# Performance work log

Hardware: AMD Instinct MI355X
Metric: run time of the kernel (lower is better)

Reference implementation:

```python
import jax, jax.numpy as jnp
import numpy as np

B, N, C = 2, 2048, 1024
H, D = 16, 64
SEQ_DROPOUT = 0.4
K_KEEP = int(N * (1.0 - SEQ_DROPOUT))  # 1228 kept keys per (b, h)


def setup_inputs() -> dict:
    key = jax.random.key(0)
    k1, k2, k3, k4, k5 = jax.random.split(key, 5)
    x = jax.random.normal(k1, (B, N, C), dtype=jnp.float32)
    W_qkv = jax.random.normal(k2, (3 * H * D, C), dtype=jnp.float32) * 0.02
    W_out = jax.random.normal(k3, (C, H * D), dtype=jnp.float32) * 0.02
    pos_bias = jax.random.normal(k4, (H, N, N), dtype=jnp.float32) * 0.1
    seq_mask = jax.random.randint(k5, (B, H, N), 0, 10, dtype=jnp.int32)
    mask = jnp.zeros((B, N), dtype=bool)  # True = padded / masked out
    return {"x": x, "W_qkv": W_qkv, "W_out": W_out, "pos_bias": pos_bias,
            "seq_mask": seq_mask, "mask": mask}


def reference(x, W_qkv, W_out, pos_bias, seq_mask, mask):
    scale = D ** -0.5
    # qkv projection: (b n (h d qkv)) -> q,k,v each [B,H,N,D]
    qkv = (x @ W_qkv.T).reshape(B, N, H, D, 3)
    q = jnp.moveaxis(qkv[..., 0], 2, 1)
    k_full = jnp.moveaxis(qkv[..., 1], 2, 1)
    v_full = jnp.moveaxis(qkv[..., 2], 2, 1)

    # random top-k key subsampling per (b, h); padded positions forced out
    sm = jnp.where(mask[:, None, :], jnp.int32(-1), seq_mask)
    _, idx = jax.lax.top_k(sm, K_KEEP)              # [B,H,K]
    idx = jnp.sort(idx, axis=-1)

    kk = jnp.take_along_axis(k_full, idx[..., None], axis=2)  # [B,H,K,D]
    vv = jnp.take_along_axis(v_full, idx[..., None], axis=2)
    k_mask = jnp.take_along_axis(jnp.broadcast_to(mask[:, None, :], (B, H, N)), idx, axis=-1)

    dots = jnp.einsum('bhid,bhjd->bhij', q, kk) * scale       # [B,H,N,K]
    # gather position bias columns at kept key indices
    pb = jnp.take_along_axis(pos_bias[None], idx[:, :, None, :], axis=-1)  # [B,H,N,K]
    dots = dots + pb

    qk_mask = jnp.logical_and(mask[:, None, :, None], k_mask[:, :, None, :])
    causal = idx[:, :, None, :] > jnp.arange(N)[None, None, :, None]
    qk_mask = jnp.logical_or(qk_mask, causal)

    dots = jnp.where(qk_mask, -jnp.finfo(dots.dtype).max, dots)
    attn = jax.nn.softmax(dots, axis=-1)
    out = jnp.einsum('bhij,bhjd->bhid', attn, vv)             # [B,H,N,D]
    out = jnp.moveaxis(out, 1, 2).reshape(B, N, H * D)
    return out @ W_out.T
```

## Files before the change

kernel.cpp:

```cpp
#include <hip/hip_runtime.h>
#include <hip/hip_bf16.h>
#include <float.h>

#define BB    2
#define NSEQ  2048
#define CDIM  1024
#define HH    16
#define DD    64
#define KKEEP 1228

typedef __attribute__((ext_vector_type(8))) short short8_t;
typedef __attribute__((ext_vector_type(4))) short short4_t;
typedef __attribute__((ext_vector_type(4))) float f32x4;
typedef __attribute__((ext_vector_type(16))) float f32x16;
typedef __attribute__((ext_vector_type(4))) float float4_t;
typedef __attribute__((ext_vector_type(4))) unsigned uint4_t;
typedef __bf16 bf16x8 __attribute__((ext_vector_type(8)));

#define Z16 ((f32x16){0.f,0.f,0.f,0.f,0.f,0.f,0.f,0.f,0.f,0.f,0.f,0.f,0.f,0.f,0.f,0.f})

static __device__ __forceinline__ short f2bf(float x) {
  __hip_bfloat16 h = __float2bfloat16(x);
  short s;
  __builtin_memcpy(&s, &h, 2);
  return s;
}

static __device__ __forceinline__ float bf2f(short s) {
  unsigned u = ((unsigned)(unsigned short)s) << 16;
  float f;
  __builtin_memcpy(&f, &u, 4);
  return f;
}

static __device__ __forceinline__ f32x4 mfma16(bf16x8 a, bf16x8 b, f32x4 c) {
  return __builtin_amdgcn_mfma_f32_16x16x32_bf16(a, b, c, 0, 0, 0);
}

static __device__ __forceinline__ f32x16 mfma32(bf16x8 a, bf16x8 b, f32x16 c) {
  return __builtin_amdgcn_mfma_f32_32x32x16_bf16(a, b, c, 0, 0, 0);
}

static __device__ __forceinline__ void gll16(const void* g, void* l) {
  __builtin_amdgcn_global_load_lds((const __attribute__((address_space(1))) void*)g,
                                   (__attribute__((address_space(3))) void*)l,
                                   16, 0, 0);
}

__global__ __launch_bounds__(256) void cast_f32_bf16_kernel(
    const float* __restrict__ src, short* __restrict__ dst, int n4) {
  int i = blockIdx.x * 256 + threadIdx.x;
  if (i >= n4) return;
  float4_t v = ((const float4_t*)src)[i];
  short4_t o;
  o[0] = f2bf(v[0]); o[1] = f2bf(v[1]); o[2] = f2bf(v[2]); o[3] = f2bf(v[3]);
  ((short4_t*)dst)[i] = o;
}

__global__ __launch_bounds__(256) void cast_wqkv_kernel(
    const float* __restrict__ w, short* __restrict__ dst) {
  int rr = blockIdx.x;
  int c = rr >> 10, hd = rr & 1023;
  int h = hd >> 6, d = hd & 63;
  int srow = h * 192 + d * 3 + c;
  int col = threadIdx.x * 4;
  float4_t v = *(const float4_t*)(w + (size_t)srow * CDIM + col);
  short4_t o;
  o[0] = f2bf(v[0]); o[1] = f2bf(v[1]); o[2] = f2bf(v[2]); o[3] = f2bf(v[3]);
  *(short4_t*)(dst + (size_t)rr * CDIM + col) = o;
}

template <int EPI>
__global__ __launch_bounds__(256) void gemm_bt_kernel(
    const short* __restrict__ A, const short* __restrict__ B, int K, int N,
    float* __restrict__ outF, short* __restrict__ outQ,
    short* __restrict__ outK, short* __restrict__ outV) {
  __shared__ __align__(16) short lA[128 * 32];
  __shared__ __align__(16) short lB[128 * 32];
  int m0 = blockIdx.y * 128, n0 = blockIdx.x * 128;
  int tid = threadIdx.x, lane = tid & 63;
  int w = tid >> 6;
  int lq = lane & 15, lg = lane >> 4;
  int wm = w >> 1, wn = w & 1;

  f32x4 acc[4][4];
#pragma unroll
  for (int m = 0; m < 4; ++m)
#pragma unroll
    for (int n = 0; n < 4; ++n) acc[m][n] = (f32x4){0.f, 0.f, 0.f, 0.f};

  const int c0 = tid, c1 = tid + 256;
  const short* Ar0 = A + (size_t)(m0 + (c0 >> 2)) * K + (c0 & 3) * 8;
  const short* Ar1 = A + (size_t)(m0 + (c1 >> 2)) * K + (c1 & 3) * 8;
  const short* Br0 = B + (size_t)(n0 + (c0 >> 2)) * K + (c0 & 3) * 8;
  const short* Br1 = B + (size_t)(n0 + (c1 >> 2)) * K + (c1 & 3) * 8;

  for (int k0 = 0; k0 < K; k0 += 32) {
    gll16(Ar0 + k0, lA + c0 * 8);
    gll16(Ar1 + k0, lA + c1 * 8);
    gll16(Br0 + k0, lB + c0 * 8);
    gll16(Br1 + k0, lB + c1 * 8);
    __syncthreads();
    bf16x8 af[4], bf[4];
#pragma unroll
    for (int m = 0; m < 4; ++m)
      af[m] = *(const bf16x8*)(lA + (wm * 64 + m * 16 + lq) * 32 + lg * 8);
#pragma unroll
    for (int n = 0; n < 4; ++n)
      bf[n] = *(const bf16x8*)(lB + (wn * 64 + n * 16 + lq) * 32 + lg * 8);
#pragma unroll
    for (int m = 0; m < 4; ++m)
#pragma unroll
      for (int n = 0; n < 4; ++n) acc[m][n] = mfma16(af[m], bf[n], acc[m][n]);
    __syncthreads();
  }

#pragma unroll
  for (int m = 0; m < 4; ++m)
#pragma unroll
    for (int n = 0; n < 4; ++n) {
      int row_b = m0 + wm * 64 + m * 16 + lg * 4;
      int col = n0 + wn * 64 + n * 16 + lq;
#pragma unroll
      for (int r = 0; r < 4; ++r) {
        float v = acc[m][n][r];
        int row = row_b + r;
        if constexpr (EPI == 1) {
          outF[(size_t)row * N + col] = v;
        } else {
          int c = col >> 10, cc = col & 1023;
          int bb2 = row >> 11, nn = row & 2047;
          int hh2 = cc >> 6, dd2 = cc & 63;
          short val = f2bf(v);
          if (c == 0)
            outQ[((size_t)(bb2 * HH + hh2) * NSEQ + nn) * DD + dd2] = val;
          else if (c == 1)
            outK[((size_t)(bb2 * HH + hh2) * NSEQ + nn) * DD + dd2] = val;
          else
            outV[((size_t)(bb2 * HH + hh2) * DD + dd2) * NSEQ + nn] = val;
        }
      }
    }
}

__global__ __launch_bounds__(256) void topk_kernel(const int* __restrict__ seq_mask,
                                                   unsigned* __restrict__ keepw,
                                                   int* __restrict__ jminb) {
  __shared__ int hist[10];
  __shared__ int vals[NSEQ];
  __shared__ int seqc[256];
  __shared__ unsigned wbuf[64];
  __shared__ int sT, sNeed, sMin;
  int bh = blockIdx.x, tid = threadIdx.x;
  if (tid < 10) hist[tid] = 0;
  if (tid < 64) wbuf[tid] = 0;
  if (tid == 0) sMin = NSEQ;
  __syncthreads();
  const int* sm = seq_mask + (size_t)bh * NSEQ;
  for (int i = tid; i < NSEQ; i += 256) {
    int v = sm[i];
    vals[i] = v;
    atomicAdd(&hist[v], 1);
  }
  __syncthreads();
  if (tid == 0) {
    int cum = 0, t = 0;
    for (int v = 9; v >= 0; --v) {
      int hv = hist[v];
      if (cum + hv >= KKEEP) { t = v; break; }
      cum += hv;
    }
    sT = t;
    sNeed = KKEEP - cum;
  }
  __syncthreads();
  int t = sT, need = sNeed;
  int base = tid * 8, leq = 0;
  int lv[8];
#pragma unroll
  for (int j = 0; j < 8; ++j) {
    lv[j] = vals[base + j];
    leq += (lv[j] == t);
  }
  seqc[tid] = leq;
  __syncthreads();
  for (int off = 1; off < 256; off <<= 1) {
    int a = 0;
    if (tid >= off) a = seqc[tid - off];
    __syncthreads();
    seqc[tid] += a;
    __syncthreads();
  }
  int eqp = seqc[tid] - leq;
  unsigned mybits = 0;
#pragma unroll
  for (int j = 0; j < 8; ++j) {
    int v = lv[j];
    bool kept = (v > t) || (v == t && eqp < need);
    if (v == t) eqp++;
    if (kept) mybits |= (1u << j);
  }
  atomicOr(&wbuf[tid >> 2], mybits << ((tid & 3) * 8));
  if (mybits) atomicMin(&sMin, base + __ffs(mybits) - 1);
  __syncthreads();
  if (tid < 64) keepw[(size_t)bh * 64 + tid] = wbuf[tid];
  if (tid == 0) jminb[bh] = sMin;
}

#define PBLOAD(SUF, T)                                                         \
  do {                                                                         \
    const float* pb_ = pbrow + (T) * 32 + hi4;                                 \
    pbg0##SUF = *(const float4_t*)(pb_);                                       \
    pbg1##SUF = *(const float4_t*)(pb_ + 8);                                   \
    pbg2##SUF = *(const float4_t*)(pb_ + 16);                                  \
    pbg3##SUF = *(const float4_t*)(pb_ + 24);                                  \
    kw##SUF = kwp[T];                                                          \
  } while (0)

#define CHUNK32(SUF, OSUF, T)                                                  \
  do {                                                                         \
    int kb0c = (T) * 32;                                                       \
    const short* kp_ = kb_bh + (size_t)(kb0c + lq32) * DD + hi8;               \
    bf16x8 k0 = *(const bf16x8*)(kp_);                                         \
    bf16x8 k1 = *(const bf16x8*)(kp_ + 16);                                    \
    bf16x8 k2 = *(const bf16x8*)(kp_ + 32);                                    \
    bf16x8 k3 = *(const bf16x8*)(kp_ + 48);                                    \
    const short* vp0_ = vT0 + kb0c + hi8;                                      \
    const short* vp1_ = vT1 + kb0c + hi8;                                      \
    bf16x8 v00 = *(const bf16x8*)(vp0_);                                       \
    bf16x8 v01 = *(const bf16x8*)(vp0_ + 16);                                  \
    bf16x8 v10 = *(const bf16x8*)(vp1_);                                       \
    bf16x8 v11 = *(const bf16x8*)(vp1_ + 16);                                  \
    if ((T) + 1 < t1) PBLOAD(OSUF, (T) + 1);                                   \
    f32x16 s = Z16;                                                            \
    s = mfma32(k0, qf0, s);                                                    \
    s = mfma32(k1, qf1, s);                                                    \
    s = mfma32(k2, qf2, s);                                                    \
    s = mfma32(k3, qf3, s);                                                    \
    float sv[16];                                                              \
    unsigned vb = 0;                                                           \
    float cm = -FLT_MAX;                                                       \
    _Pragma("unroll") for (int g = 0; g < 4; ++g) {                            \
      float4_t pbg = (g == 0) ? pbg0##SUF : (g == 1) ? pbg1##SUF               \
                   : (g == 2) ? pbg2##SUF : pbg3##SUF;                         \
      _Pragma("unroll") for (int m = 0; m < 4; ++m) {                          \
        int rr = g * 4 + m;                                                    \
        int kk = m + g * 8 + hi4;                                              \
        int jj = kb0c + kk;                                                    \
        unsigned keep = (kw##SUF >> kk) & 1u;                                  \
        float x = (keep && jj <= qglob) ? fmaf(s[rr], 0.125f, pbg[m])          \
                                        : -FLT_MAX;                            \
        vb |= keep << rr;                                                      \
        sv[rr] = x;                                                            \
        cm = fmaxf(cm, x);                                                     \
      }                                                                        \
    }                                                                          \
    if (__any(cm > mrun)) {                     \
      float rm = fmaxf(cm, __shfl_xor(cm, 32));                                \
      float mnew = fmaxf(mrun, rm);                                            \
      float fsc = __expf(mrun - mnew);                                         \
      mrun = mnew;                                                             \
      lsum *= fsc;                                                             \
      _Pragma("unroll") for (int rr = 0; rr < 16; ++rr) {                      \
        int qr = (rr & 3) + 8 * (rr >> 2) + hi4;                               \
        float fr = __shfl(fsc, qr);                                            \
        o0[rr] *= fr;                                                          \
        o1[rr] *= fr;                                                          \
      }                                                                        \
    }                                                                          \
    float pv[16];                                                              \
    float psum = 0.f;                                                          \
    _Pragma("unroll") for (int rr = 0; rr < 16; ++rr) {                        \
      float p_ = ((vb >> rr) & 1u) ? __expf(sv[rr] - mrun) : 0.f;              \
      pv[rr] = p_;                                                             \
      psum += p_;                                                              \
    }                                                                          \
    lsum += psum;                                                              \
    unsigned w0_, w1_, w2_, w3_, w4_, w5_, w6_, w7_;                           \
    asm("v_cvt_pk_bf16_f32 %0, %1, %2" : "=v"(w0_) : "v"(pv[0]), "v"(pv[1]));  \
    asm("v_cvt_pk_bf16_f32 %0, %1, %2" : "=v"(w1_) : "v"(pv[2]), "v"(pv[3]));  \
    asm("v_cvt_pk_bf16_f32 %0, %1, %2" : "=v"(w2_) : "v"(pv[4]), "v"(pv[5]));  \
    asm("v_cvt_pk_bf16_f32 %0, %1, %2" : "=v"(w3_) : "v"(pv[6]), "v"(pv[7]));  \
    asm("v_cvt_pk_bf16_f32 %0, %1, %2" : "=v"(w4_) : "v"(pv[8]), "v"(pv[9]));  \
    asm("v_cvt_pk_bf16_f32 %0, %1, %2" : "=v"(w5_) : "v"(pv[10]), "v"(pv[11]));\
    asm("v_cvt_pk_bf16_f32 %0, %1, %2" : "=v"(w6_) : "v"(pv[12]), "v"(pv[13]));\
    asm("v_cvt_pk_bf16_f32 %0, %1, %2" : "=v"(w7_) : "v"(pv[14]), "v"(pv[15]));\
       \
    asm("v_permlane32_swap_b32 %0, %1" : "+v"(w0_), "+v"(w2_));                \
    asm("v_permlane32_swap_b32 %0, %1" : "+v"(w1_), "+v"(w3_));                \
    asm("v_permlane32_swap_b32 %0, %1" : "+v"(w4_), "+v"(w6_));                \
    asm("v_permlane32_swap_b32 %0, %1" : "+v"(w5_), "+v"(w7_));                \
    uint4_t u0_ = {w0_, w1_, w2_, w3_};                                        \
    uint4_t u1_ = {w4_, w5_, w6_, w7_};                                        \
    bf16x8 pf0 = __builtin_bit_cast(bf16x8, u0_);                              \
    bf16x8 pf1 = __builtin_bit_cast(bf16x8, u1_);                              \
    o0 = mfma32(pf0, v00, o0);                                                 \
    o0 = mfma32(pf1, v01, o0);                                                 \
    o1 = mfma32(pf0, v10, o1);                                                 \
    o1 = mfma32(pf1, v11, o1);                                                 \
  } while (0)

__global__ __launch_bounds__(128) void attn_split_kernel(
    const short* __restrict__ qb, const short* __restrict__ kb,
    const short* __restrict__ vT, const unsigned* __restrict__ keepw,
    const int* __restrict__ jminb, const float* __restrict__ pos_bias,
    short* __restrict__ Opart, float* __restrict__ mlb,
    short* __restrict__ attn_out) {
  int w = threadIdx.x >> 6, lane = threadIdx.x & 63;
  int lq32 = lane & 31, hi = lane >> 5;
  int hi4 = hi * 4, hi8 = hi * 8;
  int gid = blockIdx.x * 2 + w;
  int bh = gid & 31;
  int r = gid >> 5;
  int jmin = jminb[bh];

  int tau, part, t0, t1;
  bool big;
  if (r < 32) {
    tau = 63 - r; part = 0; t0 = 0; t1 = 32; big = true;
  } else if (r < 34) {
    tau = 0; part = r - 32;
    int nkb = (jmin > 0) ? 64 : 1;
    int half = nkb >> 1;
    t0 = part ? half : 0;
    t1 = part ? nkb : half;
    big = true;
  } else if (r < 66) {
    tau = 63 - (r - 34); part = 1; t0 = 32; t1 = tau + 1; big = true;
  } else {
    tau = 31 - (r - 66); part = 0; t0 = 0;
    t1 = (tau * 32 < jmin) ? 64 : tau + 1;
    big = false;
  }
  int stile = (tau == 0) ? 32 : (tau - 32);
  int b = bh >> 4, h = bh & 15;
  int q0 = tau << 5;
  int qglob = q0 + lq32;

  const short* qp_ = qb + ((size_t)bh * NSEQ + qglob) * DD + hi8;
  bf16x8 qf0 = *(const bf16x8*)(qp_);
  bf16x8 qf1 = *(const bf16x8*)(qp_ + 16);
  bf16x8 qf2 = *(const bf16x8*)(qp_ + 32);
  bf16x8 qf3 = *(const bf16x8*)(qp_ + 48);

  const short* kb_bh = kb + (size_t)bh * NSEQ * DD;
  const short* vT0 = vT + ((size_t)bh * DD + lq32) * NSEQ;
  const short* vT1 = vT + ((size_t)bh * DD + 32 + lq32) * NSEQ;
  const float* pbrow = pos_bias + ((size_t)h * NSEQ + qglob) * NSEQ;
  const unsigned* kwp = keepw + (size_t)bh * 64;

  float mrun = -FLT_MAX, lsum = 0.f;
  f32x16 o0 = Z16, o1 = Z16;

  float4_t pbg0A, pbg1A, pbg2A, pbg3A, pbg0B, pbg1B, pbg2B, pbg3B;
  unsigned kwA, kwB;

  if (t0 < t1) {
    PBLOAD(A, t0);
    int t = t0;
    for (;;) {
      CHUNK32(A, B, t);
      if (++t >= t1) break;
      CHUNK32(B, A, t);
      if (++t >= t1) break;
    }
  }

  float ltot = lsum + __shfl_xor(lsum, 32);

  if (big) {
    int sidx = ((bh * 33 + stile) << 1) + part;
    if (hi == 0) {
      mlb[(size_t)sidx * 64 + lq32] = mrun;
      mlb[(size_t)sidx * 64 + 32 + lq32] = ltot;
    }
    short* op = Opart + (size_t)sidx * 2048;
#pragma unroll
    for (int rr = 0; rr < 16; ++rr) {
      int qr = (rr & 3) + 8 * (rr >> 2) + hi4;
      op[qr * 64 + lq32]      = f2bf(o0[rr]);
      op[qr * 64 + 32 + lq32] = f2bf(o1[rr]);
    }
  } else {
    float inv = 1.f / ltot;
    short* ob = attn_out + ((size_t)b * NSEQ + q0) * CDIM + h * DD + lq32;
#pragma unroll
    for (int rr = 0; rr < 16; ++rr) {
      int qr = (rr & 3) + 8 * (rr >> 2) + hi4;
      float ir = __shfl(inv, qr);
      short* orow = ob + (size_t)qr * CDIM;
      orow[0]  = f2bf(o0[rr] * ir);
      orow[32] = f2bf(o1[rr] * ir);
    }
  }
}

__global__ __launch_bounds__(64) void combine_kernel(
    const float* __restrict__ mlb, const short* __restrict__ Opart,
    short* __restrict__ attn_out) {
  int blk = blockIdx.x;
  int bh = blk & 31, st = blk >> 5;
  int tau = (st < 32) ? (st + 32) : 0;
  int b = bh >> 4, h = bh & 15;
  int lane = threadIdx.x;
  int q = lane >> 1, d0 = (lane & 1) * 32;
  int p0 = (bh * 33 + st) << 1, p1 = p0 + 1;
  float m0 = mlb[(size_t)p0 * 64 + q], l0 = mlb[(size_t)p0 * 64 + 32 + q];
  float m1 = mlb[(size_t)p1 * 64 + q], l1 = mlb[(size_t)p1 * 64 + 32 + q];
  float M = fmaxf(m0, m1);
  float f0 = __expf(m0 - M), f1 = __expf(m1 - M);
  float L = l0 * f0 + l1 * f1;
  float inv = 1.f / L;
  const short* q0p = Opart + (size_t)p0 * 2048 + q * 64 + d0;
  const short* q1p = Opart + (size_t)p1 * 2048 + q * 64 + d0;
  short* orow = attn_out + ((size_t)b * NSEQ + tau * 32 + q) * CDIM + h * DD + d0;
#pragma unroll
  for (int c = 0; c < 4; ++c) {
    short8_t x0 = *(const short8_t*)(q0p + c * 8);
    short8_t x1 = *(const short8_t*)(q1p + c * 8);
    short8_t oo;
#pragma unroll
    for (int jj = 0; jj < 8; ++jj) {
      float a = bf2f(x0[jj]) * f0 + bf2f(x1[jj]) * f1;
      oo[jj] = f2bf(a * inv);
    }
    *(short8_t*)(orow + c * 8) = oo;
  }
}

extern "C" void kernel_launch(void* const* d_in, const int* in_sizes, int n_in,
                              void* d_out, int out_size, void* d_ws, size_t ws_size,
                              hipStream_t stream) {
  const float* x        = (const float*)d_in[0];
  const float* Wqkv     = (const float*)d_in[1];
  const float* Wout     = (const float*)d_in[2];
  const float* pos_bias = (const float*)d_in[3];
  const int*   seq_mask = (const int*)d_in[4];
  float* out = (float*)d_out;

  char* ws = (char*)d_ws;
  short* qb    = (short*)(ws);
  short* kbuf  = (short*)(ws + ((size_t)8  << 20));
  short* vTb   = (short*)(ws + ((size_t)16 << 20));
  short* woutb = (short*)(ws + ((size_t)24 << 20));
  short* xb    = (short*)(ws + ((size_t)26 << 20));
  short* aob   = (short*)(ws + ((size_t)26 << 20));
  short* wqkvb = (short*)(ws + ((size_t)34 << 20));
  short* Opart = (short*)(ws + ((size_t)34 << 20));
  float* mlb   = (float*)(ws + ((size_t)43 << 20));
  unsigned* keepw = (unsigned*)(ws + ((size_t)44 << 20));
  int* jminb   = (int*)(ws + ((size_t)44 << 20) + 65536);

  cast_f32_bf16_kernel<<<4096, 256, 0, stream>>>(x, xb, (BB * NSEQ * CDIM) / 4);
  cast_wqkv_kernel<<<3072, 256, 0, stream>>>(Wqkv, wqkvb);
  cast_f32_bf16_kernel<<<1024, 256, 0, stream>>>(Wout, woutb, (CDIM * HH * DD) / 4);

  gemm_bt_kernel<0><<<dim3(24, 32), 256, 0, stream>>>(xb, wqkvb, CDIM, 3 * HH * DD,
                                                      nullptr, qb, kbuf, vTb);

  topk_kernel<<<BB * HH, 256, 0, stream>>>(seq_mask, keepw, jminb);

  attn_split_kernel<<<1552, 128, 0, stream>>>(qb, kbuf, vTb, keepw, jminb,
                                              pos_bias, Opart, mlb, aob);

  combine_kernel<<<1056, 64, 0, stream>>>(mlb, Opart, aob);

  gemm_bt_kernel<1><<<dim3(8, 32), 256, 0, stream>>>(aob, woutb, HH * DD, CDIM,
                                                     out, nullptr, nullptr, nullptr);
}
```

Baseline: 209.0 us.

## Pre-swizzle K/V into MFMA fragment layout and rebalance split-K attention partitions

The QKV GEMM epilogue now writes K and V straight into a per-32-key-chunk layout that matches the MFMA operand fragments, so attention loads become contiguous per-lane 16-byte reads. Attention work is also re-split: each query tile is cut into 2–4 key partitions depending on its causal length, giving 2848 more even work items instead of a mix of big and small ones. Every tile now goes through a generalized combine kernel that merges up to 4 partials. This adds more partial-output traffic and a combine pass over all tiles, in exchange for better load balance and coalesced loads.

```diff
diff --git a/kernel.cpp b/kernel.cpp
--- a/kernel.cpp
+++ b/kernel.cpp
@@ -46,6 +46,14 @@
                                    (__attribute__((address_space(3))) void*)l,
                                    16, 0, 0);
 }
+
+static __device__ __forceinline__ int soff(int tau) {
+  if (tau == 0) return 0;
+  if (tau < 32) return 4 + (tau - 1) * 2;
+  if (tau < 48) return 66 + (tau - 32) * 3;
+  return 114 + (tau - 48) * 4;
+}
+#define SLOTS_PER_BH 178
 
 __global__ __launch_bounds__(256) void cast_f32_bf16_kernel(
     const float* __restrict__ src, short* __restrict__ dst, int n4) {
@@ -131,13 +139,20 @@
           int c = col >> 10, cc = col & 1023;
           int bb2 = row >> 11, nn = row & 2047;
           int hh2 = cc >> 6, dd2 = cc & 63;
+          int bh = bb2 * HH + hh2;
           short val = f2bf(v);
-          if (c == 0)
-            outQ[((size_t)(bb2 * HH + hh2) * NSEQ + nn) * DD + dd2] = val;
-          else if (c == 1)
-            outK[((size_t)(bb2 * HH + hh2) * NSEQ + nn) * DD + dd2] = val;
-          else
-            outV[((size_t)(bb2 * HH + hh2) * DD + dd2) * NSEQ + nn] = val;
+          if (c == 0) {
+            outQ[((size_t)bh * NSEQ + nn) * DD + dd2] = val;
+          } else if (c == 1) {
+            int t = nn >> 5, s = dd2 >> 4;
+            int lane2 = (nn & 31) | ((dd2 & 8) << 2);
+            outK[(((size_t)bh * 64 + t) * 4 + s) * 512 + lane2 * 8 + (dd2 & 7)] = val;
+          } else {
+            int t = nn >> 5;
+            int c4 = (dd2 >> 5) * 2 + ((nn >> 4) & 1);
+            int lane2 = (dd2 & 31) | ((nn & 8) << 2);
+            outV[(((size_t)bh * 64 + t) * 4 + c4) * 512 + lane2 * 8 + (nn & 7)] = val;
+          }
         }
       }
     }
@@ -220,17 +235,16 @@
 #define CHUNK32(SUF, OSUF, T)                                                  \
   do {                                                                         \
     int kb0c = (T) * 32;                                                       \
-    const short* kp_ = kb_bh + (size_t)(kb0c + lq32) * DD + hi8;               \
-    bf16x8 k0 = *(const bf16x8*)(kp_);                                         \
-    bf16x8 k1 = *(const bf16x8*)(kp_ + 16);                                    \
-    bf16x8 k2 = *(const bf16x8*)(kp_ + 32);                                    \
-    bf16x8 k3 = *(const bf16x8*)(kp_ + 48);                                    \
-    const short* vp0_ = vT0 + kb0c + hi8;                                      \
-    const short* vp1_ = vT1 + kb0c + hi8;                                      \
-    bf16x8 v00 = *(const bf16x8*)(vp0_);                                       \
-    bf16x8 v01 = *(const bf16x8*)(vp0_ + 16);                                  \
-    bf16x8 v10 = *(const bf16x8*)(vp1_);                                       \
-    bf16x8 v11 = *(const bf16x8*)(vp1_ + 16);                                  \
+    const short* kc_ = pkb + (size_t)(T) * 2048 + lane * 8;                    \
+    bf16x8 k0 = *(const bf16x8*)(kc_);                                         \
+    bf16x8 k1 = *(const bf16x8*)(kc_ + 512);                                   \
+    bf16x8 k2 = *(const bf16x8*)(kc_ + 1024);                                  \
+    bf16x8 k3 = *(const bf16x8*)(kc_ + 1536);                                  \
+    const short* vc_ = pvb + (size_t)(T) * 2048 + lane * 8;                    \
+    bf16x8 v00 = *(const bf16x8*)(vc_);                                        \
+    bf16x8 v01 = *(const bf16x8*)(vc_ + 512);                                  \
+    bf16x8 v10 = *(const bf16x8*)(vc_ + 1024);                                 \
+    bf16x8 v11 = *(const bf16x8*)(vc_ + 1536);                                 \
     if ((T) + 1 < t1) PBLOAD(OSUF, (T) + 1);                                   \
     f32x16 s = Z16;                                                            \
     s = mfma32(k0, qf0, s);                                                    \
@@ -285,7 +299,6 @@
     asm("v_cvt_pk_bf16_f32 %0, %1, %2" : "=v"(w5_) : "v"(pv[10]), "v"(pv[11]));\
     asm("v_cvt_pk_bf16_f32 %0, %1, %2" : "=v"(w6_) : "v"(pv[12]), "v"(pv[13]));\
     asm("v_cvt_pk_bf16_f32 %0, %1, %2" : "=v"(w7_) : "v"(pv[14]), "v"(pv[15]));\
-       \
     asm("v_permlane32_swap_b32 %0, %1" : "+v"(w0_), "+v"(w2_));                \
     asm("v_permlane32_swap_b32 %0, %1" : "+v"(w1_), "+v"(w3_));                \
     asm("v_permlane32_swap_b32 %0, %1" : "+v"(w4_), "+v"(w6_));                \
@@ -301,41 +314,29 @@
   } while (0)
 
 __global__ __launch_bounds__(128) void attn_split_kernel(
-    const short* __restrict__ qb, const short* __restrict__ kb,
-    const short* __restrict__ vT, const unsigned* __restrict__ keepw,
+    const short* __restrict__ qb, const short* __restrict__ PK,
+    const short* __restrict__ PV, const unsigned* __restrict__ keepw,
     const int* __restrict__ jminb, const float* __restrict__ pos_bias,
-    short* __restrict__ Opart, float* __restrict__ mlb,
-    short* __restrict__ attn_out) {
+    short* __restrict__ Opart, float* __restrict__ mlb) {
   int w = threadIdx.x >> 6, lane = threadIdx.x & 63;
   int lq32 = lane & 31, hi = lane >> 5;
   int hi4 = hi * 4, hi8 = hi * 8;
   int gid = blockIdx.x * 2 + w;
   int bh = gid & 31;
   int r = gid >> 5;
-  int jmin = jminb[bh];
-
-  int tau, part, t0, t1;
-  bool big;
-  if (r < 32) {
-    tau = 63 - r; part = 0; t0 = 0; t1 = 32; big = true;
-  } else if (r < 34) {
-    tau = 0; part = r - 32;
-    int nkb = (jmin > 0) ? 64 : 1;
-    int half = nkb >> 1;
-    t0 = part ? half : 0;
-    t1 = part ? nkb : half;
-    big = true;
-  } else if (r < 66) {
-    tau = 63 - (r - 34); part = 1; t0 = 32; t1 = tau + 1; big = true;
-  } else {
-    tau = 31 - (r - 66); part = 0; t0 = 0;
-    t1 = (tau * 32 < jmin) ? 64 : tau + 1;
-    big = false;
-  }
-  int stile = (tau == 0) ? 32 : (tau - 32);
-  int b = bh >> 4, h = bh & 15;
+  int tau, part;
+  if (r < 64)       { tau = 63 - (r >> 2); part = r & 3; }
+  else if (r < 112) { int rr = r - 64; tau = 47 - rr / 3; part = rr % 3; }
+  else if (r < 116) { tau = 0; part = r - 112; }
+  else              { int rr = r - 116; tau = 31 - (rr >> 1); part = rr & 1; }
+  int P = (tau == 0 || tau >= 48) ? 4 : (tau >= 32) ? 3 : 2;
+
+  int h = bh & 15;
   int q0 = tau << 5;
   int qglob = q0 + lq32;
+  int jmin = jminb[bh];
+  int nkb = (q0 < jmin) ? 64 : (tau + 1);
+  int t0 = (nkb * part) / P, t1 = (nkb * (part + 1)) / P;
 
   const short* qp_ = qb + ((size_t)bh * NSEQ + qglob) * DD + hi8;
   bf16x8 qf0 = *(const bf16x8*)(qp_);
@@ -343,9 +344,8 @@
   bf16x8 qf2 = *(const bf16x8*)(qp_ + 32);
   bf16x8 qf3 = *(const bf16x8*)(qp_ + 48);
 
-  const short* kb_bh = kb + (size_t)bh * NSEQ * DD;
-  const short* vT0 = vT + ((size_t)bh * DD + lq32) * NSEQ;
-  const short* vT1 = vT + ((size_t)bh * DD + 32 + lq32) * NSEQ;
+  const short* pkb = PK + (size_t)bh * 131072;
+  const short* pvb = PV + (size_t)bh * 131072;
   const float* pbrow = pos_bias + ((size_t)h * NSEQ + qglob) * NSEQ;
   const unsigned* kwp = keepw + (size_t)bh * 64;
 
@@ -368,30 +368,17 @@
 
   float ltot = lsum + __shfl_xor(lsum, 32);
 
-  if (big) {
-    int sidx = ((bh * 33 + stile) << 1) + part;
-    if (hi == 0) {
-      mlb[(size_t)sidx * 64 + lq32] = mrun;
-      mlb[(size_t)sidx * 64 + 32 + lq32] = ltot;
-    }
-    short* op = Opart + (size_t)sidx * 2048;
-#pragma unroll
-    for (int rr = 0; rr < 16; ++rr) {
-      int qr = (rr & 3) + 8 * (rr >> 2) + hi4;
-      op[qr * 64 + lq32]      = f2bf(o0[rr]);
-      op[qr * 64 + 32 + lq32] = f2bf(o1[rr]);
-    }
-  } else {
-    float inv = 1.f / ltot;
-    short* ob = attn_out + ((size_t)b * NSEQ + q0) * CDIM + h * DD + lq32;
-#pragma unroll
-    for (int rr = 0; rr < 16; ++rr) {
-      int qr = (rr & 3) + 8 * (rr >> 2) + hi4;
-      float ir = __shfl(inv, qr);
-      short* orow = ob + (size_t)qr * CDIM;
-      orow[0]  = f2bf(o0[rr] * ir);
-      orow[32] = f2bf(o1[rr] * ir);
-    }
+  int sidx = bh * SLOTS_PER_BH + soff(tau) + part;
+  if (hi == 0) {
+    mlb[(size_t)sidx * 64 + lq32] = mrun;
+    mlb[(size_t)sidx * 64 + 32 + lq32] = ltot;
+  }
+  short* op = Opart + (size_t)sidx * 2048;
+#pragma unroll
+  for (int rr = 0; rr < 16; ++rr) {
+    int qr = (rr & 3) + 8 * (rr >> 2) + hi4;
+    op[qr * 64 + lq32]      = f2bf(o0[rr]);
+    op[qr * 64 + 32 + lq32] = f2bf(o1[rr]);
   }
 }
 
@@ -399,31 +386,40 @@
     const float* __restrict__ mlb, const short* __restrict__ Opart,
     short* __restrict__ attn_out) {
   int blk = blockIdx.x;
-  int bh = blk & 31, st = blk >> 5;
-  int tau = (st < 32) ? (st + 32) : 0;
+  int bh = blk & 31, tau = blk >> 5;
+  int P = (tau == 0 || tau >= 48) ? 4 : (tau >= 32) ? 3 : 2;
+  int s0 = bh * SLOTS_PER_BH + soff(tau);
   int b = bh >> 4, h = bh & 15;
   int lane = threadIdx.x;
   int q = lane >> 1, d0 = (lane & 1) * 32;
-  int p0 = (bh * 33 + st) << 1, p1 = p0 + 1;
-  float m0 = mlb[(size_t)p0 * 64 + q], l0 = mlb[(size_t)p0 * 64 + 32 + q];
-  float m1 = mlb[(size_t)p1 * 64 + q], l1 = mlb[(size_t)p1 * 64 + 32 + q];
-  float M = fmaxf(m0, m1);
-  float f0 = __expf(m0 - M), f1 = __expf(m1 - M);
-  float L = l0 * f0 + l1 * f1;
+
+  float m[4], l[4];
+  float M = -FLT_MAX;
+  for (int p = 0; p < P; ++p) {
+    m[p] = mlb[(size_t)(s0 + p) * 64 + q];
+    l[p] = mlb[(size_t)(s0 + p) * 64 + 32 + q];
+    M = fmaxf(M, m[p]);
+  }
+  float f[4];
+  float L = 0.f;
+  for (int p = 0; p < P; ++p) {
+    f[p] = __expf(m[p] - M);
+    L += l[p] * f[p];
+  }
   float inv = 1.f / L;
-  const short* q0p = Opart + (size_t)p0 * 2048 + q * 64 + d0;
-  const short* q1p = Opart + (size_t)p1 * 2048 + q * 64 + d0;
+
   short* orow = attn_out + ((size_t)b * NSEQ + tau * 32 + q) * CDIM + h * DD + d0;
 #pragma unroll
   for (int c = 0; c < 4; ++c) {
-    short8_t x0 = *(const short8_t*)(q0p + c * 8);
-    short8_t x1 = *(const short8_t*)(q1p + c * 8);
+    float acc[8] = {0.f, 0.f, 0.f, 0.f, 0.f, 0.f, 0.f, 0.f};
+    for (int p = 0; p < P; ++p) {
+      short8_t x = *(const short8_t*)(Opart + (size_t)(s0 + p) * 2048 + q * 64 + d0 + c * 8);
+#pragma unroll
+      for (int jj = 0; jj < 8; ++jj) acc[jj] += f[p] * bf2f(x[jj]);
+    }
     short8_t oo;
 #pragma unroll
-    for (int jj = 0; jj < 8; ++jj) {
-      float a = bf2f(x0[jj]) * f0 + bf2f(x1[jj]) * f1;
-      oo[jj] = f2bf(a * inv);
-    }
+    for (int jj = 0; jj < 8; ++jj) oo[jj] = f2bf(acc[jj] * inv);
     *(short8_t*)(orow + c * 8) = oo;
   }
 }
@@ -440,30 +436,30 @@
 
   char* ws = (char*)d_ws;
   short* qb    = (short*)(ws);
-  short* kbuf  = (short*)(ws + ((size_t)8  << 20));
-  short* vTb   = (short*)(ws + ((size_t)16 << 20));
+  short* PK    = (short*)(ws + ((size_t)8  << 20));
+  short* PV    = (short*)(ws + ((size_t)16 << 20));
   short* woutb = (short*)(ws + ((size_t)24 << 20));
   short* xb    = (short*)(ws + ((size_t)26 << 20));
-  short* aob   = (short*)(ws + ((size_t)26 << 20));
   short* wqkvb = (short*)(ws + ((size_t)34 << 20));
-  short* Opart = (short*)(ws + ((size_t)34 << 20));
-  float* mlb   = (float*)(ws + ((size_t)43 << 20));
-  unsigned* keepw = (unsigned*)(ws + ((size_t)44 << 20));
-  int* jminb   = (int*)(ws + ((size_t)44 << 20) + 65536);
+  short* Opart = (short*)(ws + ((size_t)26 << 20));
+  float* mlb   = (float*)(ws + ((size_t)495 << 17));
+  short* aob   = (short*)(ws + ((size_t)51 << 20));
+  unsigned* keepw = (unsigned*)(ws + ((size_t)59 << 20) + (512 << 10));
+  int* jminb   = (int*)(ws + ((size_t)59 << 20) + (512 << 10) + 65536);
 
   cast_f32_bf16_kernel<<<4096, 256, 0, stream>>>(x, xb, (BB * NSEQ * CDIM) / 4);
   cast_wqkv_kernel<<<3072, 256, 0, stream>>>(Wqkv, wqkvb);
   cast_f32_bf16_kernel<<<1024, 256, 0, stream>>>(Wout, woutb, (CDIM * HH * DD) / 4);
 
   gemm_bt_kernel<0><<<dim3(24, 32), 256, 0, stream>>>(xb, wqkvb, CDIM, 3 * HH * DD,
-                                                      nullptr, qb, kbuf, vTb);
+                                                      nullptr, qb, PK, PV);
 
   topk_kernel<<<BB * HH, 256, 0, stream>>>(seq_mask, keepw, jminb);
 
-  attn_split_kernel<<<1552, 128, 0, stream>>>(qb, kbuf, vTb, keepw, jminb,
-                                              pos_bias, Opart, mlb, aob);
-
-  combine_kernel<<<1056, 64, 0, stream>>>(mlb, Opart, aob);
+  attn_split_kernel<<<2848, 128, 0, stream>>>(qb, PK, PV, keepw, jminb,
+                                              pos_bias, Opart, mlb);
+
+  combine_kernel<<<2048, 64, 0, stream>>>(mlb, Opart, aob);
 
   gemm_bt_kernel<1><<<dim3(8, 32), 256, 0, stream>>>(aob, woutb, HH * DD, CDIM,
                                                      out, nullptr, nullptr, nullptr);
```

Result: faster. 178.7 us (-14.5%).
